# Kernel optimization log

Measured on AMD Instinct MI355X. Metric: run time of the kernel, lower is better.

## Reference

```python
import jax, jax.numpy as jnp
import numpy as np

DIM = 256
NH = 8
KA = 3
DR = 4
CR = DIM // DR            # 64 reduced dim
CPH = CR // NH            # 8 channels per head
SCALE = (DIM // NH) ** -0.5  # head_dim uses full dim, per original code


def _unfold_kernel():
    # fixed identity depthwise kernel: out channel c*KA*KA+i picks window offset i of channel c
    eye = jnp.eye(KA * KA, dtype=jnp.float32).reshape(KA * KA, 1, KA, KA)
    return jnp.tile(eye, (CPH, 1, 1, 1))  # (KA*KA*CPH, 1, KA, KA)


def _dwconv(x, w, b):
    # x: (N, CPH, H, W), w: (KA*KA*CPH, 1, KA, KA), groups=CPH, 'same' zero padding
    y = jax.lax.conv_general_dilated(
        x, w, window_strides=(1, 1), padding=[(KA // 2, KA // 2)] * 2,
        dimension_numbers=("NCHW", "OIHW", "NCHW"), feature_group_count=CPH)
    return y + b[None, :, None, None]


def setup_inputs() -> dict:
    key = jax.random.key(0)
    ks = jax.random.split(key, 8)
    B, L = 16, 4096
    x = jax.random.normal(ks[0], (B, L, DIM), dtype=jnp.float32)
    qkv_w = jax.random.normal(ks[1], (3 * CR, DIM), dtype=jnp.float32) * 0.02
    qkv_b = jnp.zeros((3 * CR,), dtype=jnp.float32)
    dep_conv_b = jax.random.normal(ks[2], (KA * KA * CPH,), dtype=jnp.float32) * 0.02
    dep_conv1_w = jax.random.normal(ks[3], (KA * KA * CPH, 1, KA, KA), dtype=jnp.float32) * 0.02
    dep_conv1_b = jnp.zeros((KA * KA * CPH,), dtype=jnp.float32)
    rpb_table = jax.random.normal(ks[4], (1, NH, 1, KA * KA, 1, 1), dtype=jnp.float32) * 0.02
    proj_w = jax.random.normal(ks[5], (DIM, CR), dtype=jnp.float32) * 0.02
    proj_b = jnp.zeros((DIM,), dtype=jnp.float32)
    return {
        "x": x, "H22": 64, "W22": 64,
        "relative_pos_index": jax.random.randint(ks[6], (9, 9), 0, 9),
        "relative_coords_table": jax.random.normal(ks[7], (9, 2), dtype=jnp.float32),
        "qkv_w": qkv_w, "qkv_b": qkv_b,
        "dep_conv_b": dep_conv_b, "dep_conv1_w": dep_conv1_w, "dep_conv1_b": dep_conv1_b,
        "rpb_table": rpb_table, "proj_w": proj_w, "proj_b": proj_b,
    }


def reference(x, H22, W22, relative_pos_index, relative_coords_table,
              qkv_w, qkv_b, dep_conv_b, dep_conv1_w, dep_conv1_b,
              rpb_table, proj_w, proj_b):
    B1, L1, C1 = x.shape
    H = int(np.sqrt(L1)); W = H
    # faithful to original: reshape (B,L,C)->(B,C,H,W) then move channels last
    xhw = x.reshape(B1, C1, H, W).transpose(0, 2, 3, 1)       # (B,H,W,C)
    qkv = xhw @ qkv_w.T + qkv_b                               # (B,H,W,3*CR)
    f = qkv.transpose(0, 3, 1, 2).reshape(B1 * NH, 3 * CPH, H, W)
    q = (f[:, :CPH] * SCALE).reshape(B1, NH, CPH, 1, H, W)
    kk = f[:, CPH:2 * CPH]                                    # (B*NH, CPH, H, W)
    vv = f[:, 2 * CPH:]
    w0 = _unfold_kernel()
    k = _dwconv(kk, w0, dep_conv_b) + _dwconv(kk, dep_conv1_w, dep_conv1_b)
    v = _dwconv(vv, w0, dep_conv_b) + _dwconv(vv, dep_conv1_w, dep_conv1_b)
    k = k.reshape(B1, NH, CPH, KA * KA, H, W) + rpb_table     # rpb bias on k
    v = v.reshape(B1, NH, CPH, KA * KA, H, W)
    attn = jax.nn.softmax((q * k).sum(2, keepdims=True), axis=3)  # (B,NH,1,ka*ka,H,W)
    out = (attn * v).sum(3).reshape(B1, CR, H, W).transpose(0, 2, 3, 1)  # (B,H,W,CR)
    out = out @ proj_w.T + proj_b                              # (B,H,W,C1)
    return out.transpose(0, 3, 1, 2).reshape(B1, L1, C1)
```

## Files before the change

kernel.cpp:

```cpp
#include <hip/hip_runtime.h>

#define BB 16
#define HW 4096
#define DIMC 256
#define NHEAD 8
#define CPH 8
#define NQKV 192
#define SCALE 0.17677669529663687f

typedef __attribute__((ext_vector_type(8))) short bf16x8;
typedef __attribute__((ext_vector_type(4))) float f32x4;

__device__ inline unsigned short f2b(float f) {
  union { float f; unsigned int u; } x; x.f = f;
  unsigned int r = x.u + 0x7FFFu + ((x.u >> 16) & 1u);
  return (unsigned short)(r >> 16);
}
__device__ inline float b2f(unsigned short u) {
  union { unsigned int u; float f; } x; x.u = ((unsigned int)u) << 16;
  return x.f;
}
__device__ inline void async_copy16(const void* g, void* l) {
  __builtin_amdgcn_global_load_lds((const __attribute__((address_space(1))) void*)g,
                                   (__attribute__((address_space(3))) void*)l, 16, 0, 0);
}

__global__ __launch_bounds__(256) void cast_xT(const float* __restrict__ x,
                                               unsigned short* __restrict__ xT) {
  __shared__ float Xs[64][69];
  const int b = blockIdx.z;
  const int k0 = blockIdx.y * 64;
  const int s0 = blockIdx.x * 64;
  const int tid = threadIdx.x;
  const float* xb = x + (size_t)b * (DIMC * HW);
#pragma unroll
  for (int i = 0; i < 4; ++i) {
    int idx = tid + i * 256;
    int kr = idx >> 4, f = idx & 15;
    float4 v = *(const float4*)&xb[(size_t)(k0 + kr) * HW + s0 + f * 4];
    Xs[kr][f * 4 + 0] = v.x; Xs[kr][f * 4 + 1] = v.y;
    Xs[kr][f * 4 + 2] = v.z; Xs[kr][f * 4 + 3] = v.w;
  }
  __syncthreads();
  unsigned short* ob = xT + (size_t)b * (HW * DIMC);
#pragma unroll
  for (int i = 0; i < 2; ++i) {
    int slot = tid + i * 256;
    int sr = slot >> 3, g8 = slot & 7;
    unsigned short pk[8];
#pragma unroll
    for (int j = 0; j < 8; ++j) pk[j] = f2b(Xs[g8 * 8 + j][sr]);
    *(uint4*)&ob[(size_t)(s0 + sr) * DIMC + k0 + g8 * 8] = *(uint4*)pk;
  }
}

__global__ __launch_bounds__(256) void cast_all(const float* __restrict__ qw,
                                                unsigned short* __restrict__ qwf,
                                                const float* __restrict__ dcb,
                                                const float* __restrict__ w1,
                                                const float* __restrict__ dc1b,
                                                const float* __restrict__ rpb,
                                                float* __restrict__ prep,
                                                const float* __restrict__ pw,
                                                unsigned short* __restrict__ pwf) {
  if (blockIdx.x == 24) {
    for (int e = threadIdx.x; e < 1056; e += 256) {
      float v = 0.f;
      if (e < 864) {
        int cp = e / 12, rs = e - cp * 12;
        if (rs < 9) v = w1[cp * 9 + rs] + ((cp % 9) == rs ? 1.f : 0.f);
      } else if (e < 960) {
        int i = e - 864; int c = i / 12, p = i - c * 12;
        if (p < 9) v = dcb[c * 9 + p] + dc1b[c * 9 + p];
      } else {
        int i = e - 960; int n = i / 12, p = i - n * 12;
        if (p < 9) v = rpb[n * 9 + p];
      }
      prep[e] = v;
    }
    return;
  }
  if (blockIdx.x >= 25) {
    int t = (blockIdx.x - 25) * 256 + threadIdx.x;
    int lane = t & 63;
    int cell = t >> 6;
    int m = lane & 15, g = lane >> 4;
    int band = cell >> 1, c32 = cell & 1;
    int d = band * 16 + m;
    int j = c32 * 32 + g * 8;
    unsigned short pk[8];
#pragma unroll
    for (int i = 0; i < 8; ++i) pk[i] = f2b(pw[d * 64 + j + i]);
    *(uint4*)&pwf[(size_t)t * 8] = *(uint4*)pk;
    return;
  }
  int t = blockIdx.x * 256 + threadIdx.x;
  int lane = t & 63;
  int cell = t >> 6;
  int m = lane & 15, g = lane >> 4;
  int band = cell >> 3, c32 = cell & 7;
  int j = band * 16 + m;
  int k = c32 * 32 + g * 8;
  unsigned short pk[8];
#pragma unroll
  for (int i = 0; i < 8; ++i) pk[i] = f2b(qw[j * 256 + k + i]);
  *(uint4*)&qwf[(size_t)t * 8] = *(uint4*)pk;
}

__global__ __launch_bounds__(256) void qkv_mfma(const unsigned short* __restrict__ xT,
                                                const unsigned short* __restrict__ qwf,
                                                const float* __restrict__ qb,
                                                unsigned short* __restrict__ qkvt) {
  __shared__ unsigned short Bs[128 * 256];
  const int b = blockIdx.y;
  const int s_blk = blockIdx.x * 128;
  const int tid = threadIdx.x;
  const int wave = tid >> 6, lane = tid & 63;

  {
    const int row_in = lane >> 5, cst = lane & 31;
#pragma unroll
    for (int ii = 0; ii < 16; ++ii) {
      int i = wave * 16 + ii;
      int s_row = 2 * i + row_in;
      int mem_chunk = (cst & 24) | ((cst ^ s_row) & 7);
      const unsigned short* src =
          xT + ((size_t)b * HW + s_blk + s_row) * DIMC + mem_chunk * 8;
      async_copy16(src, (char*)Bs + i * 1024);
    }
  }
  __syncthreads();

  f32x4 acc[3][8];
#pragma unroll
  for (int t = 0; t < 3; ++t)
#pragma unroll
    for (int st = 0; st < 8; ++st) acc[t][st] = (f32x4){0.f, 0.f, 0.f, 0.f};

  const int n = lane & 15, g = lane >> 4;
#pragma unroll
  for (int c32 = 0; c32 < 8; ++c32) {
    bf16x8 af[3];
#pragma unroll
    for (int t = 0; t < 3; ++t) {
      int band = wave * 3 + t;
      af[t] = *(const bf16x8*)(qwf + ((size_t)(band * 8 + c32) * 64 + lane) * 8);
    }
#pragma unroll
    for (int st = 0; st < 8; ++st) {
      int s_row = st * 16 + n;
      int mc = c32 * 4 + g;
      int stc = (mc & 24) | ((mc ^ s_row) & 7);
      bf16x8 bf = *(const bf16x8*)&Bs[s_row * 256 + stc * 8];
#pragma unroll
      for (int t = 0; t < 3; ++t)
        acc[t][st] = __builtin_amdgcn_mfma_f32_16x16x32_bf16(af[t], bf, acc[t][st], 0, 0, 0);
    }
  }

  unsigned short* ob = qkvt + (size_t)b * (NQKV * HW);
#pragma unroll
  for (int t = 0; t < 3; ++t) {
    int j0 = (wave * 3 + t) * 16 + g * 4;
#pragma unroll
    for (int st = 0; st < 8; ++st) {
      int s = s_blk + st * 16 + n;
#pragma unroll
      for (int r = 0; r < 4; ++r) {
        float v = acc[t][st][r] + qb[j0 + r];
        ob[(size_t)(j0 + r) * HW + s] = f2b(v);
      }
    }
  }
}

__global__ __launch_bounds__(512, 4) void attn_proj(const unsigned short* __restrict__ qkvt,
                                                    const float* __restrict__ prep,
                                                    const unsigned short* __restrict__ pwf,
                                                    const float* __restrict__ pb,
                                                    float* __restrict__ out) {
  __shared__ float2 hal2[16][6][21];
  __shared__ __align__(16) float wA[8][108];
  __shared__ float Kbs[8][8][12];
  __shared__ float Vbs[8][12];
  __shared__ float2 Qs2[8][73];
  __shared__ unsigned short Ao[128][64];

  const int b = blockIdx.x;
  const int tile = blockIdx.y;
  const int h0 = (tile >> 2) * 8, w0 = (tile & 3) * 16;
  const int tid = threadIdx.x;
  const int w = tid >> 6, lane = tid & 63;
  const int c = lane & 7;
  const int pi = lane >> 3;
  const int pidx = w * 8 + pi;
  const int pr = pidx >> 4, pc = pidx & 15;
  const unsigned short* fbase = qkvt + (size_t)b * (NQKV * HW);

  for (int e = tid; e < 864; e += 512) ((float*)wA)[e] = prep[e];
  if (tid < 96) {
    int cc = tid / 12, p = tid - cc * 12;
    Vbs[cc][p] = prep[864 + tid];
  }
  for (int e = tid; e < 768; e += 512) {
    int nn = e / 96, r = e - nn * 96;
    int p = r % 12;
    Kbs[nn][r / 12][p] = prep[864 + r] + prep[960 + nn * 12 + p];
  }

  for (int n = 0; n < 8; ++n) {
    const unsigned short* fb = fbase + (size_t)n * 24 * HW;
    __syncthreads();

    {
      int cq = tid >> 6, px = tid & 63;
      int sp = (h0 + (px >> 4)) * 64 + w0 + (px & 15);
      float v0 = b2f(fb[(size_t)cq * HW + sp]);
      float v1 = b2f(fb[(size_t)cq * HW + sp + 256]);
      Qs2[cq][px] = make_float2(SCALE * v0, SCALE * v1);
    }
    for (int e = tid; e < 2880; e += 512) {
      int cb = e / 180;
      int rem = e - cb * 180;
      int y = rem / 18, xx = rem - y * 18;
      int gy = h0 - 1 + y, gx = w0 - 1 + xx;
      float v = 0.f;
      if ((unsigned)gy < 64u && (unsigned)gx < 64u)
        v = b2f(fb[(size_t)(8 + cb) * HW + gy * 64 + gx]);
      if (y < 6) hal2[cb][y][xx].x = v;
      if (y >= 4) hal2[cb][y - 4][xx].y = v;
    }
    __syncthreads();

    const float* wAc = &wA[c][0];
    const float2 qc = Qs2[c][pidx];
    const float* Kbn = &Kbs[n][c][0];

    float ax[9], ay[9];
    {
      float2 t[9];
#pragma unroll
      for (int dy = 0; dy < 3; ++dy)
#pragma unroll
        for (int dx = 0; dx < 3; ++dx)
          t[dy * 3 + dx] = hal2[c][pr + dy][pc + dx];
#pragma unroll
      for (int p = 0; p < 9; ++p) {
        float base = Kbn[p];
        float kx = base, ky = base;
#pragma unroll
        for (int rs = 0; rs < 9; ++rs) {
          float a = wAc[p * 12 + rs];
          kx = fmaf(a, t[rs].x, kx);
          ky = fmaf(a, t[rs].y, ky);
        }
        float lx = qc.x * kx;
        float lyv = qc.y * ky;
        lx += __shfl_xor(lx, 1);  lyv += __shfl_xor(lyv, 1);
        lx += __shfl_xor(lx, 2);  lyv += __shfl_xor(lyv, 2);
        lx += __shfl_xor(lx, 4);  lyv += __shfl_xor(lyv, 4);
        ax[p] = lx; ay[p] = lyv;
      }
    }

    {
      float mx = -1e30f, my = -1e30f;
#pragma unroll
      for (int p = 0; p < 9; ++p) { mx = fmaxf(mx, ax[p]); my = fmaxf(my, ay[p]); }
      float dx = 0.f, dy = 0.f;
#pragma unroll
      for (int p = 0; p < 9; ++p) {
        ax[p] = __expf(ax[p] - mx); dx += ax[p];
        ay[p] = __expf(ay[p] - my); dy += ay[p];
      }
      float ix = 1.f / dx, iy = 1.f / dy;
#pragma unroll
      for (int p = 0; p < 9; ++p) { ax[p] *= ix; ay[p] *= iy; }
    }

    {
      float2 t[9];
#pragma unroll
      for (int dy = 0; dy < 3; ++dy)
#pragma unroll
        for (int dx = 0; dx < 3; ++dx)
          t[dy * 3 + dx] = hal2[8 + c][pr + dy][pc + dx];
      float ocx = 0.f, ocy = 0.f;
#pragma unroll
      for (int p = 0; p < 9; ++p) {
        float base = Vbs[c][p];
        float vx = base, vy = base;
#pragma unroll
        for (int rs = 0; rs < 9; ++rs) {
          float a = wAc[p * 12 + rs];
          vx = fmaf(a, t[rs].x, vx);
          vy = fmaf(a, t[rs].y, vy);
        }
        ocx = fmaf(ax[p], vx, ocx);
        ocy = fmaf(ay[p], vy, ocy);
      }
      int col = ((n ^ (pidx & 7)) << 3) + c;
      Ao[pidx][col] = f2b(ocx);
      Ao[pidx + 64][col] = f2b(ocy);
    }
  }
  __syncthreads();

  f32x4 acc[2][8];
#pragma unroll
  for (int t = 0; t < 2; ++t)
#pragma unroll
    for (int st = 0; st < 8; ++st) acc[t][st] = (f32x4){0.f, 0.f, 0.f, 0.f};

  const int nn = lane & 15, g = lane >> 4;
#pragma unroll
  for (int c32 = 0; c32 < 2; ++c32) {
    bf16x8 af[2];
#pragma unroll
    for (int t = 0; t < 2; ++t) {
      int band = w * 2 + t;
      af[t] = *(const bf16x8*)(pwf + ((size_t)(band * 2 + c32) * 64 + lane) * 8);
    }
#pragma unroll
    for (int st = 0; st < 8; ++st) {
      int s_row = st * 16 + nn;
      int stc = (c32 * 4 + g) ^ (s_row & 7);
      bf16x8 bf = *(const bf16x8*)&Ao[s_row][stc * 8];
#pragma unroll
      for (int t = 0; t < 2; ++t)
        acc[t][st] = __builtin_amdgcn_mfma_f32_16x16x32_bf16(af[t], bf, acc[t][st], 0, 0, 0);
    }
  }

  float bias[2][4];
#pragma unroll
  for (int t = 0; t < 2; ++t)
#pragma unroll
    for (int r = 0; r < 4; ++r) bias[t][r] = pb[(w * 2 + t) * 16 + g * 4 + r];

  float* ob = out + ((size_t)b << 20);
#pragma unroll
  for (int t = 0; t < 2; ++t) {
    int d0 = (w * 2 + t) * 16 + g * 4;
#pragma unroll
    for (int st = 0; st < 8; ++st) {
      int sp = (h0 + (st >> 2) * 4 + (st & 3)) * 64 + w0 + nn;
#pragma unroll
      for (int r = 0; r < 4; ++r)
        ob[(size_t)(d0 + r) * HW + sp] = acc[t][st][r] + bias[t][r];
    }
  }
}

extern "C" void kernel_launch(void* const* d_in, const int* in_sizes, int n_in,
                              void* d_out, int out_size, void* d_ws, size_t ws_size,
                              hipStream_t stream) {
  (void)in_sizes; (void)n_in; (void)out_size; (void)ws_size;
  const float* x    = (const float*)d_in[0];
  const float* qw   = (const float*)d_in[5];
  const float* qb   = (const float*)d_in[6];
  const float* dcb  = (const float*)d_in[7];
  const float* w1   = (const float*)d_in[8];
  const float* dc1b = (const float*)d_in[9];
  const float* rpb  = (const float*)d_in[10];
  const float* pw   = (const float*)d_in[11];
  const float* pb   = (const float*)d_in[12];

  unsigned short* qkvt = (unsigned short*)d_ws;
  unsigned short* qwf  = (unsigned short*)((char*)d_ws + 25165824);
  float* prep          = (float*)((char*)d_ws + 29360128);
  unsigned short* pwf  = (unsigned short*)((char*)d_ws + 30408704);
  unsigned short* xT   = (unsigned short*)((char*)d_ws + 33554432);

  cast_all<<<33, 256, 0, stream>>>(qw, qwf, dcb, w1, dc1b, rpb, prep, pw, pwf);
  cast_xT<<<dim3(64, 4, BB), 256, 0, stream>>>(x, xT);
  qkv_mfma<<<dim3(32, BB), 256, 0, stream>>>(xT, qwf, qb, qkvt);
  attn_proj<<<dim3(BB, 32), 512, 0, stream>>>(qkvt, prep, pwf, pb, (float*)d_out);
}
```

Measured before the change: 225.7 us.

## Fuse x transpose-cast into QKV GEMM and halve attention tile height

Removes the separate cast_xT kernel: qkv_mfma now reads fp32 x directly, converts to bf16 and writes the swizzled LDS tile itself, which avoids writing and re-reading a bf16 transposed copy of x. The attention kernel processes 4x16 pixel tiles instead of 8x16 (one pixel per thread instead of two), so it launches twice as many blocks with a smaller halo and smaller LDS use. The trade-offs are strided global reads of x (one float per lane per load, no vector loads) and more halo overlap across tiles.

```diff
diff --git a/kernel.cpp b/kernel.cpp
--- a/kernel.cpp
+++ b/kernel.cpp
@@ -19,39 +19,6 @@
 __device__ inline float b2f(unsigned short u) {
   union { unsigned int u; float f; } x; x.u = ((unsigned int)u) << 16;
   return x.f;
-}
-__device__ inline void async_copy16(const void* g, void* l) {
-  __builtin_amdgcn_global_load_lds((const __attribute__((address_space(1))) void*)g,
-                                   (__attribute__((address_space(3))) void*)l, 16, 0, 0);
-}
-
-__global__ __launch_bounds__(256) void cast_xT(const float* __restrict__ x,
-                                               unsigned short* __restrict__ xT) {
-  __shared__ float Xs[64][69];
-  const int b = blockIdx.z;
-  const int k0 = blockIdx.y * 64;
-  const int s0 = blockIdx.x * 64;
-  const int tid = threadIdx.x;
-  const float* xb = x + (size_t)b * (DIMC * HW);
-#pragma unroll
-  for (int i = 0; i < 4; ++i) {
-    int idx = tid + i * 256;
-    int kr = idx >> 4, f = idx & 15;
-    float4 v = *(const float4*)&xb[(size_t)(k0 + kr) * HW + s0 + f * 4];
-    Xs[kr][f * 4 + 0] = v.x; Xs[kr][f * 4 + 1] = v.y;
-    Xs[kr][f * 4 + 2] = v.z; Xs[kr][f * 4 + 3] = v.w;
-  }
-  __syncthreads();
-  unsigned short* ob = xT + (size_t)b * (HW * DIMC);
-#pragma unroll
-  for (int i = 0; i < 2; ++i) {
-    int slot = tid + i * 256;
-    int sr = slot >> 3, g8 = slot & 7;
-    unsigned short pk[8];
-#pragma unroll
-    for (int j = 0; j < 8; ++j) pk[j] = f2b(Xs[g8 * 8 + j][sr]);
-    *(uint4*)&ob[(size_t)(s0 + sr) * DIMC + k0 + g8 * 8] = *(uint4*)pk;
-  }
 }
 
 __global__ __launch_bounds__(256) void cast_all(const float* __restrict__ qw,
@@ -107,7 +74,7 @@
   *(uint4*)&qwf[(size_t)t * 8] = *(uint4*)pk;
 }
 
-__global__ __launch_bounds__(256) void qkv_mfma(const unsigned short* __restrict__ xT,
+__global__ __launch_bounds__(256) void qkv_mfma(const float* __restrict__ x,
                                                 const unsigned short* __restrict__ qwf,
                                                 const float* __restrict__ qb,
                                                 unsigned short* __restrict__ qkvt) {
@@ -116,17 +83,23 @@
   const int s_blk = blockIdx.x * 128;
   const int tid = threadIdx.x;
   const int wave = tid >> 6, lane = tid & 63;
+  const float* xb = x + (size_t)b * (DIMC * HW);
 
   {
-    const int row_in = lane >> 5, cst = lane & 31;
-#pragma unroll
-    for (int ii = 0; ii < 16; ++ii) {
-      int i = wave * 16 + ii;
-      int s_row = 2 * i + row_in;
-      int mem_chunk = (cst & 24) | ((cst ^ s_row) & 7);
-      const unsigned short* src =
-          xT + ((size_t)b * HW + s_blk + s_row) * DIMC + mem_chunk * 8;
-      async_copy16(src, (char*)Bs + i * 1024);
+    const int s_row = (wave & 1) * 64 + lane;
+    const int k_base = (wave >> 1) * 128;
+    const float* p = xb + (size_t)k_base * HW + s_blk + s_row;
+#pragma unroll
+    for (int kc = 0; kc < 16; ++kc) {
+      unsigned short pk[8];
+#pragma unroll
+      for (int j = 0; j < 8; ++j) {
+        pk[j] = f2b(*p);
+        p += HW;
+      }
+      int mc = (k_base >> 3) + kc;
+      int stc = (mc & 24) | ((mc ^ s_row) & 7);
+      *(uint4*)&Bs[s_row * 256 + stc * 8] = *(uint4*)pk;
     }
   }
   __syncthreads();
@@ -179,16 +152,16 @@
                                                     const unsigned short* __restrict__ pwf,
                                                     const float* __restrict__ pb,
                                                     float* __restrict__ out) {
-  __shared__ float2 hal2[16][6][21];
+  __shared__ float hal[16][6][20];
   __shared__ __align__(16) float wA[8][108];
   __shared__ float Kbs[8][8][12];
   __shared__ float Vbs[8][12];
-  __shared__ float2 Qs2[8][73];
-  __shared__ unsigned short Ao[128][64];
+  __shared__ float Qs[8][68];
+  __shared__ unsigned short Ao[64][64];
 
   const int b = blockIdx.x;
-  const int tile = blockIdx.y;
-  const int h0 = (tile >> 2) * 8, w0 = (tile & 3) * 16;
+  const int ty = blockIdx.y;
+  const int h0 = (ty >> 2) * 4, w0 = (ty & 3) * 16;
   const int tid = threadIdx.x;
   const int w = tid >> 6, lane = tid & 63;
   const int c = lane & 7;
@@ -215,102 +188,84 @@
     {
       int cq = tid >> 6, px = tid & 63;
       int sp = (h0 + (px >> 4)) * 64 + w0 + (px & 15);
-      float v0 = b2f(fb[(size_t)cq * HW + sp]);
-      float v1 = b2f(fb[(size_t)cq * HW + sp + 256]);
-      Qs2[cq][px] = make_float2(SCALE * v0, SCALE * v1);
-    }
-    for (int e = tid; e < 2880; e += 512) {
-      int cb = e / 180;
-      int rem = e - cb * 180;
+      Qs[cq][px] = SCALE * b2f(fb[(size_t)cq * HW + sp]);
+    }
+    for (int e = tid; e < 1728; e += 512) {
+      int cb = e / 108;
+      int rem = e - cb * 108;
       int y = rem / 18, xx = rem - y * 18;
       int gy = h0 - 1 + y, gx = w0 - 1 + xx;
       float v = 0.f;
       if ((unsigned)gy < 64u && (unsigned)gx < 64u)
         v = b2f(fb[(size_t)(8 + cb) * HW + gy * 64 + gx]);
-      if (y < 6) hal2[cb][y][xx].x = v;
-      if (y >= 4) hal2[cb][y - 4][xx].y = v;
+      hal[cb][y][xx] = v;
     }
     __syncthreads();
 
     const float* wAc = &wA[c][0];
-    const float2 qc = Qs2[c][pidx];
+    const float qc = Qs[c][pidx];
     const float* Kbn = &Kbs[n][c][0];
 
-    float ax[9], ay[9];
+    float ax[9];
     {
-      float2 t[9];
+      float t[9];
 #pragma unroll
       for (int dy = 0; dy < 3; ++dy)
 #pragma unroll
         for (int dx = 0; dx < 3; ++dx)
-          t[dy * 3 + dx] = hal2[c][pr + dy][pc + dx];
+          t[dy * 3 + dx] = hal[c][pr + dy][pc + dx];
 #pragma unroll
       for (int p = 0; p < 9; ++p) {
-        float base = Kbn[p];
-        float kx = base, ky = base;
-#pragma unroll
-        for (int rs = 0; rs < 9; ++rs) {
-          float a = wAc[p * 12 + rs];
-          kx = fmaf(a, t[rs].x, kx);
-          ky = fmaf(a, t[rs].y, ky);
-        }
-        float lx = qc.x * kx;
-        float lyv = qc.y * ky;
-        lx += __shfl_xor(lx, 1);  lyv += __shfl_xor(lyv, 1);
-        lx += __shfl_xor(lx, 2);  lyv += __shfl_xor(lyv, 2);
-        lx += __shfl_xor(lx, 4);  lyv += __shfl_xor(lyv, 4);
-        ax[p] = lx; ay[p] = lyv;
+        float kx = Kbn[p];
+#pragma unroll
+        for (int rs = 0; rs < 9; ++rs)
+          kx = fmaf(wAc[p * 12 + rs], t[rs], kx);
+        float lx = qc * kx;
+        lx += __shfl_xor(lx, 1);
+        lx += __shfl_xor(lx, 2);
+        lx += __shfl_xor(lx, 4);
+        ax[p] = lx;
       }
     }
 
     {
-      float mx = -1e30f, my = -1e30f;
-#pragma unroll
-      for (int p = 0; p < 9; ++p) { mx = fmaxf(mx, ax[p]); my = fmaxf(my, ay[p]); }
-      float dx = 0.f, dy = 0.f;
+      float mx = -1e30f;
+#pragma unroll
+      for (int p = 0; p < 9; ++p) mx = fmaxf(mx, ax[p]);
+      float dx = 0.f;
+#pragma unroll
+      for (int p = 0; p < 9; ++p) { ax[p] = __expf(ax[p] - mx); dx += ax[p]; }
+      float ix = 1.f / dx;
+#pragma unroll
+      for (int p = 0; p < 9; ++p) ax[p] *= ix;
+    }
+
+    {
+      float t[9];
+#pragma unroll
+      for (int dy = 0; dy < 3; ++dy)
+#pragma unroll
+        for (int dx = 0; dx < 3; ++dx)
+          t[dy * 3 + dx] = hal[8 + c][pr + dy][pc + dx];
+      float oc = 0.f;
 #pragma unroll
       for (int p = 0; p < 9; ++p) {
-        ax[p] = __expf(ax[p] - mx); dx += ax[p];
-        ay[p] = __expf(ay[p] - my); dy += ay[p];
-      }
-      float ix = 1.f / dx, iy = 1.f / dy;
-#pragma unroll
-      for (int p = 0; p < 9; ++p) { ax[p] *= ix; ay[p] *= iy; }
-    }
-
-    {
-      float2 t[9];
-#pragma unroll
-      for (int dy = 0; dy < 3; ++dy)
-#pragma unroll
-        for (int dx = 0; dx < 3; ++dx)
-          t[dy * 3 + dx] = hal2[8 + c][pr + dy][pc + dx];
-      float ocx = 0.f, ocy = 0.f;
-#pragma unroll
-      for (int p = 0; p < 9; ++p) {
-        float base = Vbs[c][p];
-        float vx = base, vy = base;
-#pragma unroll
-        for (int rs = 0; rs < 9; ++rs) {
-          float a = wAc[p * 12 + rs];
-          vx = fmaf(a, t[rs].x, vx);
-          vy = fmaf(a, t[rs].y, vy);
-        }
-        ocx = fmaf(ax[p], vx, ocx);
-        ocy = fmaf(ay[p], vy, ocy);
-      }
-      int col = ((n ^ (pidx & 7)) << 3) + c;
-      Ao[pidx][col] = f2b(ocx);
-      Ao[pidx + 64][col] = f2b(ocy);
+        float vx = Vbs[c][p];
+#pragma unroll
+        for (int rs = 0; rs < 9; ++rs)
+          vx = fmaf(wAc[p * 12 + rs], t[rs], vx);
+        oc = fmaf(ax[p], vx, oc);
+      }
+      Ao[pidx][((n ^ (pidx & 7)) << 3) + c] = f2b(oc);
     }
   }
   __syncthreads();
 
-  f32x4 acc[2][8];
+  f32x4 acc[2][4];
 #pragma unroll
   for (int t = 0; t < 2; ++t)
 #pragma unroll
-    for (int st = 0; st < 8; ++st) acc[t][st] = (f32x4){0.f, 0.f, 0.f, 0.f};
+    for (int st = 0; st < 4; ++st) acc[t][st] = (f32x4){0.f, 0.f, 0.f, 0.f};
 
   const int nn = lane & 15, g = lane >> 4;
 #pragma unroll
@@ -322,7 +277,7 @@
       af[t] = *(const bf16x8*)(pwf + ((size_t)(band * 2 + c32) * 64 + lane) * 8);
     }
 #pragma unroll
-    for (int st = 0; st < 8; ++st) {
+    for (int st = 0; st < 4; ++st) {
       int s_row = st * 16 + nn;
       int stc = (c32 * 4 + g) ^ (s_row & 7);
       bf16x8 bf = *(const bf16x8*)&Ao[s_row][stc * 8];
@@ -343,8 +298,8 @@
   for (int t = 0; t < 2; ++t) {
     int d0 = (w * 2 + t) * 16 + g * 4;
 #pragma unroll
-    for (int st = 0; st < 8; ++st) {
-      int sp = (h0 + (st >> 2) * 4 + (st & 3)) * 64 + w0 + nn;
+    for (int st = 0; st < 4; ++st) {
+      int sp = (h0 + st) * 64 + w0 + nn;
 #pragma unroll
       for (int r = 0; r < 4; ++r)
         ob[(size_t)(d0 + r) * HW + sp] = acc[t][st][r] + bias[t][r];
@@ -370,10 +325,8 @@
   unsigned short* qwf  = (unsigned short*)((char*)d_ws + 25165824);
   float* prep          = (float*)((char*)d_ws + 29360128);
   unsigned short* pwf  = (unsigned short*)((char*)d_ws + 30408704);
-  unsigned short* xT   = (unsigned short*)((char*)d_ws + 33554432);
 
   cast_all<<<33, 256, 0, stream>>>(qw, qwf, dcb, w1, dc1b, rpb, prep, pw, pwf);
-  cast_xT<<<dim3(64, 4, BB), 256, 0, stream>>>(x, xT);
-  qkv_mfma<<<dim3(32, BB), 256, 0, stream>>>(xT, qwf, qb, qkvt);
-  attn_proj<<<dim3(BB, 32), 512, 0, stream>>>(qkvt, prep, pwf, pb, (float*)d_out);
-}
+  qkv_mfma<<<dim3(32, BB), 256, 0, stream>>>(x, qwf, qb, qkvt);
+  attn_proj<<<dim3(BB, 64), 512, 0, stream>>>(qkvt, prep, pwf, pb, (float*)d_out);
+}
```

Result: faster. 207.0 us (-8.3%).
